# Kernel optimization log

Measured on AMD Instinct MI355X. Metric: run time of the kernel, lower is better.

## Reference

```python
import jax, jax.numpy as jnp
import numpy as np

NEG_INF = -1e30  # stands in for -inf on the H-diagonal (matches softmax zeroing)


def conv1x1(x, W, b):
    # x: [B,C,H,W], W: [O,C], b: [O] -> [B,O,H,W]
    return jnp.einsum('bchw,oc->bohw', x, W) + b[None, :, None, None]


def setup_inputs() -> dict:
    key = jax.random.key(0)
    ks = jax.random.split(key, 8)
    B, C, H, W = 4, 64, 256, 256
    C8 = C // 8
    s = 1.0 / np.sqrt(C)
    return {
        'x': jax.random.normal(ks[0], (B, C, H, W), jnp.float32),
        'Wq': jax.random.normal(ks[1], (C8, C), jnp.float32) * s,
        'bq': jnp.zeros((C8,), jnp.float32),
        'Wk': jax.random.normal(ks[2], (C8, C), jnp.float32) * s,
        'bk': jnp.zeros((C8,), jnp.float32),
        'Wv': jax.random.normal(ks[3], (C, C), jnp.float32) * s,
        'bv': jnp.zeros((C,), jnp.float32),
        'gamma': jnp.zeros((1,), jnp.float32),
    }


def reference(x, Wq, bq, Wk, bk, Wv, bv, gamma):
    B, C, H, W = x.shape
    q = conv1x1(x, Wq, bq)   # [B,C8,H,W]
    k = conv1x1(x, Wk, bk)   # [B,C8,H,W]
    v = conv1x1(x, Wv, bv)   # [B,C,H,W]

    # Row (height-axis) attention energies with -inf on the self (diagonal) entry.
    energy_H = jnp.einsum('bchw,bcjw->bhwj', q, k)               # [B,H,W,H]
    diag = jnp.eye(H, dtype=bool)[:, None, :]                    # [H,1,H]
    energy_H = jnp.where(diag[None], NEG_INF, energy_H)
    # Column (width-axis) attention energies.
    energy_W = jnp.einsum('bchw,bchj->bhwj', q, k)               # [B,H,W,W]

    att = jax.nn.softmax(jnp.concatenate([energy_H, energy_W], axis=3), axis=3)
    att_H, att_W = att[..., :H], att[..., H:]                    # [B,H,W,H], [B,H,W,W]

    out_H = jnp.einsum('bcjw,bhwj->bchw', v, att_H)
    out_W = jnp.einsum('bchj,bhwj->bchw', v, att_W)
    return gamma[0] * (out_H + out_W) + x
```

## Files before the change

kernel.cpp:

```cpp
#include <hip/hip_runtime.h>

#define Bn 4
#define Cn 64
#define Hn 256
#define Wn 256
#define HWn 65536

typedef unsigned int u32;
typedef __attribute__((ext_vector_type(2))) unsigned int u32x2;
typedef __attribute__((ext_vector_type(8))) short bf16x8;
typedef __attribute__((ext_vector_type(4))) float f32x4;
typedef __attribute__((ext_vector_type(16))) float f32x16;

__device__ __forceinline__ unsigned short f2b(float f) {
    union { float f; unsigned u; } v; v.f = f;
    return (unsigned short)(v.u >> 16);
}
__device__ __forceinline__ float b2f(unsigned short s) {
    union { float f; unsigned u; } v; v.u = ((unsigned)s) << 16;
    return v.f;
}
__device__ __forceinline__ u32 cvtpk(float lo, float hi) {
    u32 r;
    asm("v_cvt_pk_bf16_f32 %0, %1, %2" : "=v"(r) : "v"(lo), "v"(hi));
    return r;
}
__device__ __forceinline__ void vswap(u32& a, u32& b) {
    asm volatile("v_permlane32_swap_b32 %0, %1" : "+v"(a), "+v"(b));
}
__device__ __forceinline__ float pair_other(float v, int lane) {
    union { float f; u32 u; } A; A.f = v;
    u32 a = A.u, b = A.u;
    vswap(a, b);
    union { u32 u; float f; } R; R.u = (lane < 32) ? b : a;
    return R.f;
}
__device__ __forceinline__ bf16x8 buildP(const float* p) {
    u32 A = cvtpk(p[0], p[1]), B = cvtpk(p[4], p[5]);
    u32 C = cvtpk(p[2], p[3]), D = cvtpk(p[6], p[7]);
    vswap(A, B); vswap(C, D);
    union { u32 w[4]; bf16x8 v; } u;
    u.w[0] = A; u.w[1] = C; u.w[2] = B; u.w[3] = D;
    return u.v;
}

__global__ __launch_bounds__(256) void k_proj(
    const float* __restrict__ x,
    const float* __restrict__ Wq, const float* __restrict__ bq,
    const float* __restrict__ Wk, const float* __restrict__ bk,
    const float* __restrict__ Wv, const float* __restrict__ bv,
    unsigned short* __restrict__ qbr, unsigned short* __restrict__ kbr,
    unsigned short* __restrict__ v_row)
{
    __shared__ __align__(16) char Xl[16384];
    int t = threadIdx.x, lane = t & 63, wv = t >> 6;
    int bid = blockIdx.x;
    int b = bid >> 9, rest = bid & 511;
    int h = rest >> 1, half = rest & 1;
    int row16 = lane & 15, g = lane >> 4;

    const float* xb2 = x + (size_t)b * Cn * HWn + (size_t)h * Wn + half * 128;

    #pragma unroll
    for (int pass = 0; pass < 2; ++pass) {
        int px4 = (t & 31) * 4;
        int c0s = ((t >> 5) << 2) + pass * 32;
        f32x4 v0 = *(const f32x4*)(xb2 + (size_t)(c0s + 0) * HWn + px4);
        f32x4 v1 = *(const f32x4*)(xb2 + (size_t)(c0s + 1) * HWn + px4);
        f32x4 v2 = *(const f32x4*)(xb2 + (size_t)(c0s + 2) * HWn + px4);
        f32x4 v3 = *(const f32x4*)(xb2 + (size_t)(c0s + 3) * HWn + px4);
        #pragma unroll
        for (int i = 0; i < 4; ++i) {
            int px = px4 + i;
            u32x2 w;
            w[0] = (u32)f2b(v0[i]) | ((u32)f2b(v1[i]) << 16);
            w[1] = (u32)f2b(v2[i]) | ((u32)f2b(v3[i]) << 16);
            unsigned addr = (unsigned)(px * 128) + (((unsigned)(c0s * 2)) ^ ((((unsigned)px >> 3) & 7) << 4));
            *(u32x2*)(Xl + addr) = w;
        }
    }

    bf16x8 Af[5][2];
    #pragma unroll
    for (int m = 0; m < 5; ++m) {
        const float* wrow;
        if (m == 0) wrow = (row16 < 8) ? (Wq + row16 * 64) : (Wk + (row16 - 8) * 64);
        else        wrow = Wv + (size_t)((m - 1) * 16 + row16) * 64;
        #pragma unroll
        for (int ks = 0; ks < 2; ++ks) {
            int c0 = ks * 32 + g * 8;
            f32x4 w0 = *(const f32x4*)(wrow + c0);
            f32x4 w1 = *(const f32x4*)(wrow + c0 + 4);
            bf16x8 a;
            a[0] = (short)f2b(w0[0]); a[1] = (short)f2b(w0[1]);
            a[2] = (short)f2b(w0[2]); a[3] = (short)f2b(w0[3]);
            a[4] = (short)f2b(w1[0]); a[5] = (short)f2b(w1[1]);
            a[6] = (short)f2b(w1[2]); a[7] = (short)f2b(w1[3]);
            Af[m][ks] = a;
        }
    }

    f32x4 acc[5][2];
    #pragma unroll
    for (int m = 0; m < 5; ++m)
        #pragma unroll
        for (int nt = 0; nt < 2; ++nt)
            acc[m][nt] = (f32x4){0.f, 0.f, 0.f, 0.f};

    __syncthreads();

    #pragma unroll
    for (int nt = 0; nt < 2; ++nt) {
        int px = wv * 32 + nt * 16 + row16;
        #pragma unroll
        for (int ks = 0; ks < 2; ++ks) {
            int c0 = ks * 32 + g * 8;
            unsigned addr = (unsigned)(px * 128) + (((unsigned)(c0 * 2)) ^ ((((unsigned)px >> 3) & 7) << 4));
            bf16x8 bf = *(const bf16x8*)(Xl + addr);
            #pragma unroll
            for (int m = 0; m < 5; ++m)
                acc[m][nt] = __builtin_amdgcn_mfma_f32_16x16x32_bf16(Af[m][ks], bf, acc[m][nt], 0, 0, 0);
        }
    }

    f32x4 bQK = (g < 2) ? *(const f32x4*)(bq + g * 4)
                        : *(const f32x4*)(bk + (g - 2) * 4);
    #pragma unroll
    for (int nt = 0; nt < 2; ++nt) {
        int p = half * 128 + wv * 32 + nt * 16 + row16;
        f32x4 d = acc[0][nt];
        d[0] += bQK[0]; d[1] += bQK[1]; d[2] += bQK[2]; d[3] += bQK[3];
        u32 w0 = (u32)f2b(d[0]) | ((u32)f2b(d[1]) << 16);
        u32 w1 = (u32)f2b(d[2]) | ((u32)f2b(d[3]) << 16);
        size_t roff = ((size_t)(b * Hn + h) * Wn + p) * 8 + (size_t)((g & 1) * 4);
        if (g < 2) {
            *(u32*)(qbr + roff) = w0; *(u32*)(qbr + roff + 2) = w1;
        } else {
            *(u32*)(kbr + roff) = w0; *(u32*)(kbr + roff + 2) = w1;
        }
        #pragma unroll
        for (int m = 1; m < 5; ++m) {
            f32x4 bV = *(const f32x4*)(bv + (m - 1) * 16 + g * 4);
            unsigned short* vp = v_row + (size_t)b * Cn * HWn
                               + (size_t)((m - 1) * 16 + g * 4) * HWn
                               + (size_t)h * Wn + p;
            #pragma unroll
            for (int r = 0; r < 4; ++r)
                vp[(size_t)r * HWn] = f2b(acc[m][nt][r] + bV[r]);
        }
    }
}

__global__ __launch_bounds__(256) void k_tr_bf16(
    const unsigned short* __restrict__ in, unsigned short* __restrict__ out,
    int R, int Ccols)
{
    __shared__ unsigned short tile[64][66];
    int t = threadIdx.x;
    int lr = t >> 6, lc = t & 63;
    int tilesC = Ccols >> 6;
    int per_b = (R >> 6) * tilesC;
    int bid = blockIdx.x;
    int b = bid / per_b;
    int rem = bid - b * per_b;
    int r0 = (rem / tilesC) << 6;
    int c0 = (rem - (rem / tilesC) * tilesC) << 6;
    const unsigned short* ip = in + (size_t)b * R * Ccols;
    unsigned short* op = out + (size_t)b * R * Ccols;
    #pragma unroll
    for (int i = 0; i < 16; ++i) {
        int r = lr * 16 + i;
        tile[r][lc] = ip[(size_t)(r0 + r) * Ccols + c0 + lc];
    }
    __syncthreads();
    #pragma unroll
    for (int i = 0; i < 16; ++i) {
        int c = lr * 16 + i;
        op[(size_t)(c0 + c) * R + r0 + lc] = tile[lc][c];
    }
}

__global__ __launch_bounds__(256, 2) void k_attnH(
    const unsigned short* __restrict__ qbr, const unsigned short* __restrict__ kbr,
    const unsigned short* __restrict__ vT,
    unsigned short* __restrict__ ohT,
    float* __restrict__ mH, float* __restrict__ sH)
{
    __shared__ __align__(16) unsigned short Vl[16384];
    int t = threadIdx.x, lane = t & 63, wv = t >> 6;
    int l31 = lane & 31, hi = lane >> 5;
    int bid = blockIdx.x, b = bid >> 8, w = bid & 255;

    const char* vsrc = (const char*)(vT + ((size_t)(b * Wn + w)) * Cn * Hn);
    #pragma unroll
    for (int p = 0; p < 8; ++p) {
        int lin = p * 4096 + t * 16;
        int c = lin >> 9;
        f32x4 d = *(const f32x4*)(vsrc + lin);
        unsigned dst = (unsigned)lin ^ ((unsigned)(c & 7) << 4);
        *(f32x4*)((char*)Vl + dst) = d;
    }

    bf16x8 zer = {};
    bf16x8 Qf[2], Kf[8];
    #pragma unroll
    for (int qt = 0; qt < 2; ++qt) {
        int q = (wv * 2 + qt) * 32 + l31;
        bf16x8 v = *(const bf16x8*)(qbr + ((size_t)(b * Hn + q) * Wn + w) * 8);
        Qf[qt] = (hi == 0) ? v : zer;
    }
    #pragma unroll
    for (int jt = 0; jt < 8; ++jt) {
        int j = jt * 32 + l31;
        bf16x8 v = *(const bf16x8*)(kbr + ((size_t)(b * Hn + j) * Wn + w) * 8);
        Kf[jt] = (hi == 0) ? v : zer;
    }
    __syncthreads();

    #pragma unroll
    for (int qt = 0; qt < 2; ++qt) {
        int qtA = wv * 2 + qt;
        int q = qtA * 32 + l31;
        f32x16 Oa = {}, Ob = {};
        float m = -3.0e38f, s = 0.f;
        #pragma unroll
        for (int jt = 0; jt < 8; ++jt) {
            f32x16 zc = {};
            f32x16 e = __builtin_amdgcn_mfma_f32_32x32x16_bf16(Kf[jt], Qf[qt], zc, 0, 0, 0);
            if (jt == qtA) {
                #pragma unroll
                for (int r = 0; r < 16; ++r) {
                    int rl = (r & 3) + 8 * (r >> 2) + 4 * hi;
                    e[r] = (rl == l31) ? -1e30f : e[r];
                }
            }
            float pm = e[0];
            #pragma unroll
            for (int r = 1; r < 16; ++r) pm = fmaxf(pm, e[r]);
            pm = fmaxf(pm, pair_other(pm, lane));
            if (!__all(pm <= m + 8.0f)) {
                float mn = fmaxf(m, pm);
                float f = __expf(m - mn);
                #pragma unroll
                for (int r = 0; r < 16; ++r) { Oa[r] *= f; Ob[r] *= f; }
                s *= f; m = mn;
            }
            float p[16];
            float ss = 0.f;
            #pragma unroll
            for (int r = 0; r < 16; ++r) { p[r] = __expf(e[r] - m); ss += p[r]; }
            s += ss;
            bf16x8 P0 = buildP(p);
            bf16x8 P1 = buildP(p + 8);
            #pragma unroll
            for (int k2 = 0; k2 < 2; ++k2) {
                int ktA = jt * 2 + k2;
                bf16x8 Pf = k2 ? P1 : P0;
                #pragma unroll
                for (int ct = 0; ct < 2; ++ct) {
                    int c = ct * 32 + l31;
                    unsigned ad = ((unsigned)(c * 512 + ktA * 32 + hi * 16))
                                ^ ((unsigned)(c & 7) << 4);
                    bf16x8 Vf = *(const bf16x8*)((const char*)Vl + ad);
                    if (ct == 0) Oa = __builtin_amdgcn_mfma_f32_32x32x16_bf16(Vf, Pf, Oa, 0, 0, 0);
                    else         Ob = __builtin_amdgcn_mfma_f32_32x32x16_bf16(Vf, Pf, Ob, 0, 0, 0);
                }
            }
        }
        float s_tot = s + pair_other(s, lane);
        if (hi == 0) {
            size_t so = ((size_t)(b * Wn + w)) * Hn + q;
            mH[so] = m; sH[so] = s_tot;
        }
        unsigned short* ob = ohT + ((size_t)(b * Wn + w)) * Cn * Hn;
        #pragma unroll
        for (int ct = 0; ct < 2; ++ct) {
            #pragma unroll
            for (int r = 0; r < 16; ++r) {
                int c = (r & 3) + 8 * (r >> 2) + 4 * hi + ct * 32;
                float val = ct ? Ob[r] : Oa[r];
                ob[(size_t)c * Hn + q] = f2b(val);
            }
        }
    }
}

__global__ __launch_bounds__(256, 2) void k_attnW(
    const unsigned short* __restrict__ qbr, const unsigned short* __restrict__ kbr,
    const unsigned short* __restrict__ v_row,
    const unsigned short* __restrict__ oh_row,
    const float* __restrict__ mH, const float* __restrict__ sH,
    const float* __restrict__ x, const float* __restrict__ gamma,
    float* __restrict__ out)
{
    __shared__ __align__(16) unsigned short Vl[16384];
    int t = threadIdx.x, lane = t & 63, wv = t >> 6;
    int l31 = lane & 31, hi = lane >> 5;
    int bid = blockIdx.x, b = bid >> 8, h = bid & 255;

    #pragma unroll
    for (int p = 0; p < 8; ++p) {
        int lin = p * 4096 + t * 16;
        int c = lin >> 9, off = lin & 511;
        const char* src = (const char*)(v_row + ((size_t)(b * Cn + c)) * HWn + (size_t)h * Wn) + off;
        f32x4 d = *(const f32x4*)src;
        unsigned dst = (unsigned)lin ^ ((unsigned)(c & 7) << 4);
        *(f32x4*)((char*)Vl + dst) = d;
    }

    const unsigned short* qb = qbr + ((size_t)(b * Hn + h)) * Wn * 8;
    const unsigned short* kb = kbr + ((size_t)(b * Hn + h)) * Wn * 8;
    bf16x8 zer = {};
    bf16x8 Qf[2], Kf[8];
    #pragma unroll
    for (int qt = 0; qt < 2; ++qt) {
        int q = (wv * 2 + qt) * 32 + l31;
        bf16x8 v = *(const bf16x8*)(qb + (size_t)q * 8);
        Qf[qt] = (hi == 0) ? v : zer;
    }
    #pragma unroll
    for (int jt = 0; jt < 8; ++jt) {
        int j = jt * 32 + l31;
        bf16x8 v = *(const bf16x8*)(kb + (size_t)j * 8);
        Kf[jt] = (hi == 0) ? v : zer;
    }
    float g = gamma[0];
    __syncthreads();

    #pragma unroll
    for (int qt = 0; qt < 2; ++qt) {
        int q = (wv * 2 + qt) * 32 + l31;
        f32x16 Oa = {}, Ob = {};
        float m = -3.0e38f, s = 0.f;
        #pragma unroll
        for (int jt = 0; jt < 8; ++jt) {
            f32x16 zc = {};
            f32x16 e = __builtin_amdgcn_mfma_f32_32x32x16_bf16(Kf[jt], Qf[qt], zc, 0, 0, 0);
            float pm = e[0];
            #pragma unroll
            for (int r = 1; r < 16; ++r) pm = fmaxf(pm, e[r]);
            pm = fmaxf(pm, pair_other(pm, lane));
            if (!__all(pm <= m + 8.0f)) {
                float mn = fmaxf(m, pm);
                float f = __expf(m - mn);
                #pragma unroll
                for (int r = 0; r < 16; ++r) { Oa[r] *= f; Ob[r] *= f; }
                s *= f; m = mn;
            }
            float p[16];
            float ss = 0.f;
            #pragma unroll
            for (int r = 0; r < 16; ++r) { p[r] = __expf(e[r] - m); ss += p[r]; }
            s += ss;
            bf16x8 P0 = buildP(p);
            bf16x8 P1 = buildP(p + 8);
            #pragma unroll
            for (int k2 = 0; k2 < 2; ++k2) {
                int ktA = jt * 2 + k2;
                bf16x8 Pf = k2 ? P1 : P0;
                #pragma unroll
                for (int ct = 0; ct < 2; ++ct) {
                    int c = ct * 32 + l31;
                    unsigned ad = ((unsigned)(c * 512 + ktA * 32 + hi * 16))
                                ^ ((unsigned)(c & 7) << 4);
                    bf16x8 Vf = *(const bf16x8*)((const char*)Vl + ad);
                    if (ct == 0) Oa = __builtin_amdgcn_mfma_f32_32x32x16_bf16(Vf, Pf, Oa, 0, 0, 0);
                    else         Ob = __builtin_amdgcn_mfma_f32_32x32x16_bf16(Vf, Pf, Ob, 0, 0, 0);
                }
            }
        }
        float s_tot = s + pair_other(s, lane);
        size_t so = ((size_t)(b * Wn + q)) * Hn + h;
        float mh = mH[so], sh = sH[so];
        float M = fmaxf(m, mh);
        float eW = __expf(m - M), eH = __expf(mh - M);
        float inv = 1.0f / (s_tot * eW + sh * eH);
        float sI = eW * inv, sF = eH * inv;
        #pragma unroll
        for (int ct = 0; ct < 2; ++ct) {
            #pragma unroll
            for (int r = 0; r < 16; ++r) {
                int c = (r & 3) + 8 * (r >> 2) + 4 * hi + ct * 32;
                size_t idx = ((size_t)(b * Cn + c) * Hn + h) * Wn + q;
                float val = ct ? Ob[r] : Oa[r];
                out[idx] = g * (val * sI + b2f(oh_row[idx]) * sF) + x[idx];
            }
        }
    }
}

extern "C" void kernel_launch(void* const* d_in, const int* in_sizes, int n_in,
                              void* d_out, int out_size, void* d_ws, size_t ws_size,
                              hipStream_t stream) {
    const float* x  = (const float*)d_in[0];
    const float* Wq = (const float*)d_in[1];
    const float* bq = (const float*)d_in[2];
    const float* Wk = (const float*)d_in[3];
    const float* bk = (const float*)d_in[4];
    const float* Wv = (const float*)d_in[5];
    const float* bv = (const float*)d_in[6];
    const float* gm = (const float*)d_in[7];
    float* out = (float*)d_out;
    char* ws = (char*)d_ws;

    const size_t BHW = (size_t)Bn * Hn * Wn;
    unsigned short* qbr = (unsigned short*)ws;
    unsigned short* kbr = qbr + 8 * BHW;
    unsigned short* v_row = kbr + 8 * BHW;
    unsigned short* vT    = v_row + 64 * BHW;
    unsigned short* ohT   = vT + 64 * BHW;
    unsigned short* oh_row = vT;
    float* mHb = (float*)(ohT + 64 * BHW);
    float* sHb = mHb + BHW;

    k_proj<<<Bn * Hn * 2, 256, 0, stream>>>(x, Wq, bq, Wk, bk, Wv, bv,
                                            qbr, kbr, v_row);
    k_tr_bf16<<<Bn * (16384 / 64) * (256 / 64), 256, 0, stream>>>(v_row, vT, 16384, 256);
    k_attnH<<<Bn * Wn, 256, 0, stream>>>(qbr, kbr, vT, ohT, mHb, sHb);
    k_tr_bf16<<<Bn * (256 / 64) * (16384 / 64), 256, 0, stream>>>(ohT, oh_row, 256, 16384);
    k_attnW<<<Bn * Hn, 256, 0, stream>>>(qbr, kbr, v_row, oh_row, mHb, sHb, x, gm, out);
}
```

Measured before the change: 129.2 us.

## Make projection kernel persistent over four tiles with double-buffered prefetch

The projection kernel now processes four half-row units per block instead of one, launching 512 blocks rather than 2048. It double-buffers the LDS tile and prefetches the next unit's x values into registers while the current unit's MFMA and stores run. The aim is to amortise the weight-fragment setup and hide global load latency. The trade-offs are fewer blocks for latency hiding, higher register use from the prefetch staging, and twice the LDS per block.

Result: faster. 116.7 us (-9.7%).

```diff
diff --git a/kernel.cpp b/kernel.cpp
--- a/kernel.cpp
+++ b/kernel.cpp
@@ -52,33 +52,10 @@
     unsigned short* __restrict__ qbr, unsigned short* __restrict__ kbr,
     unsigned short* __restrict__ v_row)
 {
-    __shared__ __align__(16) char Xl[16384];
+    __shared__ __align__(16) char Xl[2][16384];
     int t = threadIdx.x, lane = t & 63, wv = t >> 6;
-    int bid = blockIdx.x;
-    int b = bid >> 9, rest = bid & 511;
-    int h = rest >> 1, half = rest & 1;
     int row16 = lane & 15, g = lane >> 4;
-
-    const float* xb2 = x + (size_t)b * Cn * HWn + (size_t)h * Wn + half * 128;
-
-    #pragma unroll
-    for (int pass = 0; pass < 2; ++pass) {
-        int px4 = (t & 31) * 4;
-        int c0s = ((t >> 5) << 2) + pass * 32;
-        f32x4 v0 = *(const f32x4*)(xb2 + (size_t)(c0s + 0) * HWn + px4);
-        f32x4 v1 = *(const f32x4*)(xb2 + (size_t)(c0s + 1) * HWn + px4);
-        f32x4 v2 = *(const f32x4*)(xb2 + (size_t)(c0s + 2) * HWn + px4);
-        f32x4 v3 = *(const f32x4*)(xb2 + (size_t)(c0s + 3) * HWn + px4);
-        #pragma unroll
-        for (int i = 0; i < 4; ++i) {
-            int px = px4 + i;
-            u32x2 w;
-            w[0] = (u32)f2b(v0[i]) | ((u32)f2b(v1[i]) << 16);
-            w[1] = (u32)f2b(v2[i]) | ((u32)f2b(v3[i]) << 16);
-            unsigned addr = (unsigned)(px * 128) + (((unsigned)(c0s * 2)) ^ ((((unsigned)px >> 3) & 7) << 4));
-            *(u32x2*)(Xl + addr) = w;
-        }
-    }
+    int u0 = blockIdx.x * 4;
 
     bf16x8 Af[5][2];
     #pragma unroll
@@ -100,53 +77,105 @@
         }
     }
 
-    f32x4 acc[5][2];
-    #pragma unroll
-    for (int m = 0; m < 5; ++m)
-        #pragma unroll
-        for (int nt = 0; nt < 2; ++nt)
-            acc[m][nt] = (f32x4){0.f, 0.f, 0.f, 0.f};
-
-    __syncthreads();
-
-    #pragma unroll
-    for (int nt = 0; nt < 2; ++nt) {
-        int px = wv * 32 + nt * 16 + row16;
-        #pragma unroll
-        for (int ks = 0; ks < 2; ++ks) {
-            int c0 = ks * 32 + g * 8;
-            unsigned addr = (unsigned)(px * 128) + (((unsigned)(c0 * 2)) ^ ((((unsigned)px >> 3) & 7) << 4));
-            bf16x8 bf = *(const bf16x8*)(Xl + addr);
-            #pragma unroll
-            for (int m = 0; m < 5; ++m)
-                acc[m][nt] = __builtin_amdgcn_mfma_f32_16x16x32_bf16(Af[m][ks], bf, acc[m][nt], 0, 0, 0);
-        }
-    }
-
-    f32x4 bQK = (g < 2) ? *(const f32x4*)(bq + g * 4)
-                        : *(const f32x4*)(bk + (g - 2) * 4);
-    #pragma unroll
-    for (int nt = 0; nt < 2; ++nt) {
-        int p = half * 128 + wv * 32 + nt * 16 + row16;
-        f32x4 d = acc[0][nt];
-        d[0] += bQK[0]; d[1] += bQK[1]; d[2] += bQK[2]; d[3] += bQK[3];
-        u32 w0 = (u32)f2b(d[0]) | ((u32)f2b(d[1]) << 16);
-        u32 w1 = (u32)f2b(d[2]) | ((u32)f2b(d[3]) << 16);
-        size_t roff = ((size_t)(b * Hn + h) * Wn + p) * 8 + (size_t)((g & 1) * 4);
-        if (g < 2) {
-            *(u32*)(qbr + roff) = w0; *(u32*)(qbr + roff + 2) = w1;
-        } else {
-            *(u32*)(kbr + roff) = w0; *(u32*)(kbr + roff + 2) = w1;
-        }
-        #pragma unroll
-        for (int m = 1; m < 5; ++m) {
-            f32x4 bV = *(const f32x4*)(bv + (m - 1) * 16 + g * 4);
-            unsigned short* vp = v_row + (size_t)b * Cn * HWn
-                               + (size_t)((m - 1) * 16 + g * 4) * HWn
-                               + (size_t)h * Wn + p;
-            #pragma unroll
-            for (int r = 0; r < 4; ++r)
-                vp[(size_t)r * HWn] = f2b(acc[m][nt][r] + bV[r]);
+    int px4 = (t & 31) * 4;
+    int cbase = (t >> 5) << 2;
+
+    f32x4 st[2][8];
+    {
+        int u = u0;
+        int b = u >> 9, rest = u & 511, h = rest >> 1, half = rest & 1;
+        const float* xb2 = x + (size_t)b * Cn * HWn + (size_t)h * Wn + half * 128;
+        #pragma unroll
+        for (int pass = 0; pass < 2; ++pass) {
+            int c0s = cbase + pass * 32;
+            #pragma unroll
+            for (int j = 0; j < 4; ++j)
+                st[0][pass * 4 + j] = *(const f32x4*)(xb2 + (size_t)(c0s + j) * HWn + px4);
+        }
+    }
+
+    #pragma unroll
+    for (int ui = 0; ui < 4; ++ui) {
+        int u = u0 + ui;
+        int b = u >> 9, rest = u & 511, h = rest >> 1, half = rest & 1;
+        int cur = ui & 1;
+
+        #pragma unroll
+        for (int pass = 0; pass < 2; ++pass) {
+            int c0s = cbase + pass * 32;
+            #pragma unroll
+            for (int i = 0; i < 4; ++i) {
+                int px = px4 + i;
+                u32x2 w;
+                w[0] = (u32)f2b(st[cur][pass * 4 + 0][i]) | ((u32)f2b(st[cur][pass * 4 + 1][i]) << 16);
+                w[1] = (u32)f2b(st[cur][pass * 4 + 2][i]) | ((u32)f2b(st[cur][pass * 4 + 3][i]) << 16);
+                unsigned addr = (unsigned)(px * 128)
+                              + (((unsigned)(c0s * 2)) ^ ((((unsigned)px >> 3) & 7) << 4));
+                *(u32x2*)(Xl[cur] + addr) = w;
+            }
+        }
+        __syncthreads();
+
+        if (ui < 3) {
+            int un = u + 1;
+            int bn = un >> 9, restn = un & 511, hn = restn >> 1, halfn = restn & 1;
+            const float* xb2 = x + (size_t)bn * Cn * HWn + (size_t)hn * Wn + halfn * 128;
+            #pragma unroll
+            for (int pass = 0; pass < 2; ++pass) {
+                int c0s = cbase + pass * 32;
+                #pragma unroll
+                for (int j = 0; j < 4; ++j)
+                    st[cur ^ 1][pass * 4 + j] = *(const f32x4*)(xb2 + (size_t)(c0s + j) * HWn + px4);
+            }
+        }
+
+        f32x4 acc[5][2];
+        #pragma unroll
+        for (int m = 0; m < 5; ++m)
+            #pragma unroll
+            for (int nt = 0; nt < 2; ++nt)
+                acc[m][nt] = (f32x4){0.f, 0.f, 0.f, 0.f};
+
+        #pragma unroll
+        for (int nt = 0; nt < 2; ++nt) {
+            int px = wv * 32 + nt * 16 + row16;
+            #pragma unroll
+            for (int ks = 0; ks < 2; ++ks) {
+                int c0 = ks * 32 + g * 8;
+                unsigned addr = (unsigned)(px * 128)
+                              + (((unsigned)(c0 * 2)) ^ ((((unsigned)px >> 3) & 7) << 4));
+                bf16x8 bf = *(const bf16x8*)(Xl[cur] + addr);
+                #pragma unroll
+                for (int m = 0; m < 5; ++m)
+                    acc[m][nt] = __builtin_amdgcn_mfma_f32_16x16x32_bf16(Af[m][ks], bf, acc[m][nt], 0, 0, 0);
+            }
+        }
+
+        f32x4 bQK = (g < 2) ? *(const f32x4*)(bq + g * 4)
+                            : *(const f32x4*)(bk + (g - 2) * 4);
+        #pragma unroll
+        for (int nt = 0; nt < 2; ++nt) {
+            int p = half * 128 + wv * 32 + nt * 16 + row16;
+            f32x4 d = acc[0][nt];
+            d[0] += bQK[0]; d[1] += bQK[1]; d[2] += bQK[2]; d[3] += bQK[3];
+            u32 w0 = (u32)f2b(d[0]) | ((u32)f2b(d[1]) << 16);
+            u32 w1 = (u32)f2b(d[2]) | ((u32)f2b(d[3]) << 16);
+            size_t roff = ((size_t)(b * Hn + h) * Wn + p) * 8 + (size_t)((g & 1) * 4);
+            if (g < 2) {
+                *(u32*)(qbr + roff) = w0; *(u32*)(qbr + roff + 2) = w1;
+            } else {
+                *(u32*)(kbr + roff) = w0; *(u32*)(kbr + roff + 2) = w1;
+            }
+            #pragma unroll
+            for (int m = 1; m < 5; ++m) {
+                f32x4 bV = *(const f32x4*)(bv + (m - 1) * 16 + g * 4);
+                unsigned short* vp = v_row + (size_t)b * Cn * HWn
+                                   + (size_t)((m - 1) * 16 + g * 4) * HWn
+                                   + (size_t)h * Wn + p;
+                #pragma unroll
+                for (int r = 0; r < 4; ++r)
+                    vp[(size_t)r * HWn] = f2b(acc[m][nt][r] + bV[r]);
+            }
         }
     }
 }
@@ -413,8 +442,8 @@
     float* mHb = (float*)(ohT + 64 * BHW);
     float* sHb = mHb + BHW;
 
-    k_proj<<<Bn * Hn * 2, 256, 0, stream>>>(x, Wq, bq, Wk, bk, Wv, bv,
-                                            qbr, kbr, v_row);
+    k_proj<<<512, 256, 0, stream>>>(x, Wq, bq, Wk, bk, Wv, bv,
+                                    qbr, kbr, v_row);
     k_tr_bf16<<<Bn * (16384 / 64) * (256 / 64), 256, 0, stream>>>(v_row, vT, 16384, 256);
     k_attnH<<<Bn * Wn, 256, 0, stream>>>(qbr, kbr, vT, ohT, mHb, sHb);
     k_tr_bf16<<<Bn * (256 / 64) * (16384 / 64), 256, 0, stream>>>(ohT, oh_row, 256, 16384);
```
